# Kernel tuning notes

Measured on AMD Instinct MI355X. Metric: run time of the kernel, lower is better.

The kernel has to match this reference:

```python
import jax, jax.numpy as jnp
import numpy as np

N_NODES = 100000
N_EDGES = 1600000
F_IN = 100
HEADS = 3
HEAD_DIM = 64
HIDDEN = HEADS * HEAD_DIM  # 192
NUM_GRAPHS = 128
NUM_CLASSES = 2
NEG_SLOPE_ATT = 0.2   # PyG GATConv attention leaky_relu slope
NEG_SLOPE_ACT = 0.01  # F.leaky_relu default slope


def setup_inputs() -> dict:
    key = jax.random.key(0)
    ks = jax.random.split(key, 9)
    x = jax.random.normal(ks[0], (N_NODES, F_IN), dtype=jnp.float32)
    edge_index = jax.random.randint(ks[1], (2, N_EDGES), 0, N_NODES, dtype=jnp.int64)
    batch = jnp.sort(jax.random.randint(ks[2], (N_NODES,), 0, NUM_GRAPHS, dtype=jnp.int64))
    s = 0.05
    W = jax.random.normal(ks[3], (F_IN, HIDDEN), dtype=jnp.float32) * s
    att_src = jax.random.normal(ks[4], (HEADS, HEAD_DIM), dtype=jnp.float32) * s
    att_dst = jax.random.normal(ks[5], (HEADS, HEAD_DIM), dtype=jnp.float32) * s
    bias = jax.random.normal(ks[6], (HIDDEN,), dtype=jnp.float32) * s
    cls_W = jax.random.normal(ks[7], (HIDDEN, NUM_CLASSES), dtype=jnp.float32) * s
    cls_b = jax.random.normal(ks[8], (NUM_CLASSES,), dtype=jnp.float32) * s
    return {"x": x, "edge_index": edge_index, "batch": batch, "W": W,
            "att_src": att_src, "att_dst": att_dst, "bias": bias,
            "cls_W": cls_W, "cls_b": cls_b}


def _gat_forward(x, edge_index, batch, W, att_src, att_dst, bias, cls_W, cls_b):
    N = x.shape[0]
    # PyG GATConv adds self-loops by default
    loops = jnp.arange(N, dtype=edge_index.dtype)
    src = jnp.concatenate([edge_index[0], loops])
    dst = jnp.concatenate([edge_index[1], loops])

    h = (x @ W).reshape(N, HEADS, HEAD_DIM)          # [N,H,C]
    a_src = jnp.sum(h * att_src, axis=-1)            # [N,H]
    a_dst = jnp.sum(h * att_dst, axis=-1)            # [N,H]

    e = a_src[src] + a_dst[dst]                      # [Etot,H]
    e = jax.nn.leaky_relu(e, NEG_SLOPE_ATT)

    # segment softmax over incoming edges of each destination node
    m = jax.ops.segment_max(e, dst, num_segments=N)  # [N,H]
    e = jnp.exp(e - m[dst])
    denom = jax.ops.segment_sum(e, dst, num_segments=N)
    alpha = e / denom[dst]                           # [Etot,H]

    msg = h[src] * alpha[:, :, None]                 # [Etot,H,C]
    out = jax.ops.segment_sum(msg, dst, num_segments=N).reshape(N, HIDDEN) + bias

    out = jax.nn.leaky_relu(out, NEG_SLOPE_ACT)      # F.leaky_relu (dropout inactive: eval)
    pooled = jax.ops.segment_max(out, batch, num_segments=NUM_GRAPHS)  # global_max_pool
    return pooled @ cls_W + cls_b                    # [NUM_GRAPHS, NUM_CLASSES]


def reference(x, edge_index, batch, W, att_src, att_dst, bias, cls_W, cls_b):
    return _gat_forward(x, edge_index, batch, W, att_src, att_dst, bias, cls_W, cls_b)
```

## Files before the change

kernel.cpp:

```cpp
#include <hip/hip_runtime.h>
#include <math.h>

#define N_NODES   100000
#define N_EDGES   1600000
#define ETOT      1700000
#define F_IN      100
#define HEADS     3
#define HEAD_DIM  64
#define HIDDEN    192
#define NUM_GRAPHS 128
#define NUM_CLASSES 2
#define WT_COLS   208
#define KPAD      128
#define NCHUNK    ((ETOT + 1023) / 1024)
#define DRANGE    (N_NODES / 8)
#define NGEMM     (N_NODES / 32)
#define OSTRIDE   200
#define GAGG      16
#define CAP       64
#define MWIN      40
#define MWIN_SCAT 16
#define NWIN      131
#define MEGA_GRID (NWIN * MWIN)
#define SCAT_PER_CLASS (NWIN * 2)

typedef unsigned short ushort_t;
typedef __attribute__((ext_vector_type(8))) short short8;
typedef __attribute__((ext_vector_type(4))) float floatx4;

__device__ __forceinline__ unsigned f2ord(float f) {
    unsigned u = __float_as_uint(f);
    return (u & 0x80000000u) ? ~u : (u | 0x80000000u);
}
__device__ __forceinline__ float ord2f(unsigned u) {
    return __uint_as_float((u & 0x80000000u) ? (u & 0x7fffffffu) : ~u);
}
__device__ __forceinline__ unsigned bf16rn(float f) {
    unsigned u = __float_as_uint(f);
    return (u + 0x7fffu + ((u >> 16) & 1u)) >> 16;
}
__device__ __forceinline__ int rl_i(int v, int l) {
    return __builtin_amdgcn_readlane(v, l);
}
__device__ __forceinline__ float rl_f(float v, int l) {
    return __uint_as_float((unsigned)__builtin_amdgcn_readlane((int)__float_as_uint(v), l));
}
template<int CTRL>
__device__ __forceinline__ float bfly(float v) {
    int t = __builtin_amdgcn_update_dpp(0, (int)__float_as_uint(v), CTRL, 0xF, 0xF, false);
    return v + __uint_as_float((unsigned)t);
}
#define DPP_XOR1 0xB1
#define DPP_XOR2 0x4E
#define DPP_XOR8 0x128

__global__ __launch_bounds__(256) void k_prep(
        const float* __restrict__ W, const float* __restrict__ att_src,
        const float* __restrict__ att_dst,
        ushort_t* __restrict__ WT_hi, ushort_t* __restrict__ WT_lo) {
    const int c0 = blockIdx.x * 8;
    const int t = threadIdx.x;
    __shared__ float wsv_s[F_IN * 6];
    if (c0 < HIDDEN + 6 && c0 + 8 > HIDDEN) {
        for (int p = t; p < F_IN * 6; p += 256) {
            int k = p / 6, j = p % 6;
            const float* a = (j < 3) ? att_src : att_dst;
            int hh = j % 3;
            float s = 0.f;
            for (int c = 0; c < HEAD_DIM; c++)
                s += W[k * HIDDEN + hh * HEAD_DIM + c] * a[hh * HEAD_DIM + c];
            wsv_s[p] = s;
        }
        __syncthreads();
    }
    for (int idx = t; idx < 8 * KPAD; idx += 256) {
        int col = c0 + (idx >> 7), k = idx & (KPAD - 1);
        float v = 0.f;
        if (k < F_IN) {
            if (col < HIDDEN) v = W[k * HIDDEN + col];
            else if (col < HIDDEN + 6) v = wsv_s[k * 6 + (col - HIDDEN)];
        }
        unsigned hi = bf16rn(v);
        WT_hi[col * KPAD + k] = (ushort_t)hi;
        float lo = v - __uint_as_float(hi << 16);
        WT_lo[col * KPAD + k] = (ushort_t)bf16rn(lo);
    }
}

__global__ __launch_bounds__(256) void k_mega(
        const float* __restrict__ x,
        const ushort_t* __restrict__ WT_hi, const ushort_t* __restrict__ WT_lo,
        ushort_t* __restrict__ hb,
        float* __restrict__ asrc, float* __restrict__ adst,
        const int* __restrict__ ei, int* __restrict__ count,
        int* __restrict__ srcs) {
    __shared__ ushort_t lds[32 * 136 * 2];
    const int tid = threadIdx.x;
    const int r = blockIdx.x % MWIN, w = blockIdx.x / MWIN;

    if (r < MWIN_SCAT) {
        const int cls = r & 7;
        const int ord = w * 2 + (r >> 3);
        const int dlo = cls * DRANGE, dhi = dlo + DRANGE;
        for (int chunk = ord; chunk < NCHUNK; chunk += SCAT_PER_CLASS) {
            const int base = chunk * 1024 + tid;
            int d4[4], s4[4];
#pragma unroll
            for (int q = 0; q < 4; q++) {
                int j = base + q * 256;
                if (j >= ETOT) { d4[q] = -1; s4[q] = 0; continue; }
                d4[q] = (j < N_EDGES) ? ei[N_EDGES + j] : (j - N_EDGES);
                s4[q] = (j < N_EDGES) ? ei[j] : d4[q];
            }
#pragma unroll
            for (int q = 0; q < 4; q++) {
                int d = d4[q];
                if (d < dlo || d >= dhi) continue;
                int pos = atomicAdd(&count[d], 1);
                if (pos < CAP)
                    __builtin_nontemporal_store(s4[q], &srcs[(size_t)d * CAP + pos]);
            }
        }
        return;
    }

    const int tile = w * (MWIN - MWIN_SCAT) + (r - MWIN_SCAT);
    if (tile >= NGEMM) return;
    ushort_t* xs_hi = lds;
    ushort_t* xs_lo = lds + 32 * 136;
    const int base = tile * 32;
    for (int idx = tid; idx < 32 * 14; idx += 256) {
        int row = idx / 14, u = idx % 14;
        *(unsigned*)(xs_hi + row * 136 + 100 + u * 2) = 0u;
        *(unsigned*)(xs_lo + row * 136 + 100 + u * 2) = 0u;
    }
    for (int p = tid; p < 32 * 25; p += 256) {
        int row = p / 25, q = p % 25;
        float4 v = *(const float4*)(x + (size_t)(base + row) * F_IN + q * 4);
        float vv[4] = {v.x, v.y, v.z, v.w};
        ushort_t h4[4], l4[4];
#pragma unroll
        for (int e = 0; e < 4; e++) {
            unsigned hi = bf16rn(vv[e]);
            h4[e] = (ushort_t)hi;
            float lo = vv[e] - __uint_as_float(hi << 16);
            l4[e] = (ushort_t)bf16rn(lo);
        }
        int off = row * 136 + q * 4;
        *(uint2*)(xs_hi + off) = *(uint2*)h4;
        *(uint2*)(xs_lo + off) = *(uint2*)l4;
    }
    __syncthreads();

    const int wid = tid >> 6, l = tid & 63;
    const int row16 = l & 15, g = l >> 4;
    const int NT = (wid == 3) ? 4 : 3;
    const int t0 = wid * 3;

    floatx4 acc[2][4];
#pragma unroll
    for (int m = 0; m < 2; m++)
#pragma unroll
        for (int i = 0; i < 4; i++) acc[m][i] = (floatx4)0.f;

#pragma unroll
    for (int c = 0; c < 4; c++) {
        const int ke = g * 8 + c * 32;
        short8 ah0 = *(const short8*)(xs_hi + row16 * 136 + ke);
        short8 al0 = *(const short8*)(xs_lo + row16 * 136 + ke);
        short8 ah1 = *(const short8*)(xs_hi + (16 + row16) * 136 + ke);
        short8 al1 = *(const short8*)(xs_lo + (16 + row16) * 136 + ke);
#pragma unroll
        for (int ti = 0; ti < 4; ti++) {
            if (ti >= NT) break;
            const int col = (t0 + ti) * 16 + row16;
            short8 bh = *(const short8*)(WT_hi + col * KPAD + ke);
            short8 bl = *(const short8*)(WT_lo + col * KPAD + ke);
            acc[0][ti] = __builtin_amdgcn_mfma_f32_16x16x32_bf16(ah0, bh, acc[0][ti], 0, 0, 0);
            acc[0][ti] = __builtin_amdgcn_mfma_f32_16x16x32_bf16(ah0, bl, acc[0][ti], 0, 0, 0);
            acc[0][ti] = __builtin_amdgcn_mfma_f32_16x16x32_bf16(al0, bh, acc[0][ti], 0, 0, 0);
            acc[1][ti] = __builtin_amdgcn_mfma_f32_16x16x32_bf16(ah1, bh, acc[1][ti], 0, 0, 0);
            acc[1][ti] = __builtin_amdgcn_mfma_f32_16x16x32_bf16(ah1, bl, acc[1][ti], 0, 0, 0);
            acc[1][ti] = __builtin_amdgcn_mfma_f32_16x16x32_bf16(al1, bh, acc[1][ti], 0, 0, 0);
        }
    }

    __syncthreads();

#pragma unroll
    for (int ti = 0; ti < 4; ti++) {
        if (ti >= NT) break;
        const int tile_c = t0 + ti;
        if (tile_c < 12) {
#pragma unroll
            for (int m = 0; m < 2; m++)
#pragma unroll
                for (int rr = 0; rr < 4; rr++) {
                    int node = m * 16 + g * 4 + rr;
                    lds[node * OSTRIDE + tile_c * 16 + row16] =
                        (ushort_t)bf16rn(acc[m][ti][rr]);
                }
        } else if (row16 < 6) {
#pragma unroll
            for (int m = 0; m < 2; m++)
#pragma unroll
                for (int rr = 0; rr < 4; rr++) {
                    int node = base + m * 16 + g * 4 + rr;
                    if (row16 < 3) asrc[node * HEADS + row16] = acc[m][ti][rr];
                    else           adst[node * HEADS + (row16 - 3)] = acc[m][ti][rr];
                }
        }
    }
    __syncthreads();

    uint4* hb4 = (uint4*)(hb + (size_t)base * HIDDEN);
#pragma unroll
    for (int i = 0; i < 3; i++) {
        int q = tid + i * 256;
        int row = q / 24, c8 = q % 24;
        hb4[q] = *(const uint4*)(lds + row * OSTRIDE + c8 * 8);
    }
}

#define GAT_FMA(u, a)                                         \
    do {                                                      \
        acc[0] += (a) * __uint_as_float((u).x << 16);         \
        acc[1] += (a) * __uint_as_float((u).x & 0xffff0000u); \
        acc[2] += (a) * __uint_as_float((u).y << 16);         \
        acc[3] += (a) * __uint_as_float((u).y & 0xffff0000u); \
        acc[4] += (a) * __uint_as_float((u).z << 16);         \
        acc[5] += (a) * __uint_as_float((u).z & 0xffff0000u); \
        acc[6] += (a) * __uint_as_float((u).w << 16);         \
        acc[7] += (a) * __uint_as_float((u).w & 0xffff0000u); \
        dpart += (a);                                         \
    } while (0)

__global__ __launch_bounds__(192) void k_aggr(const int* __restrict__ count,
        const int* __restrict__ srcs, const float* __restrict__ asrc,
        const float* __restrict__ adst, const ushort_t* __restrict__ hb,
        const float* __restrict__ bias, const int* __restrict__ batch,
        unsigned* __restrict__ pooled) {
    __shared__ float sm[HIDDEN];
    const int n0 = blockIdx.x * GAGG;
    const int tid = threadIdx.x;
    const int head = tid >> 6, lane = tid & 63;
    const int srci = (lane & 3) | ((lane >> 1) & 4);
    const int slot = ((lane >> 2) & 1) | ((lane >> 3) & 6);
    const char* hbase = (const char*)hb + head * 128 + slot * 16;
    const int c0 = head * HEAD_DIM + slot * 8;

    int cntv = (lane < GAGG) ? count[n0 + lane] : 0;
    int bgv  = (lane < GAGG) ? batch[n0 + lane] : 0;
    float adv = (lane < GAGG * HEADS) ? adst[n0 * HEADS + lane] : 0.f;
    float bv[8];
#pragma unroll
    for (int k = 0; k < 8; k++) bv[k] = bias[c0 + k];

    float vmax[8];
#pragma unroll
    for (int k = 0; k < 8; k++) vmax[k] = -INFINITY;
    int curg = rl_i(bgv, 0);

    int cnt_cur = rl_i(cntv, 0); if (cnt_cur > CAP) cnt_cur = CAP;
    int cntB = (GAGG > 1) ? rl_i(cntv, 1) : 0; if (cntB > CAP) cntB = CAP;
    int sA = 0, sB = 0;
    if (lane < cnt_cur)
        sA = __builtin_nontemporal_load(&srcs[(size_t)n0 * CAP + lane]);
    if (lane < cntB)
        sB = __builtin_nontemporal_load(&srcs[(size_t)(n0 + 1) * CAP + lane]);
    float aA = (lane < cnt_cur) ? asrc[sA * HEADS + head] : 0.f;

    for (int g = 0; g < GAGG; g++) {
        const int gg = rl_i(bgv, g);
        if (gg != curg) {
            if ((lane & 11) == 0) {
#pragma unroll
                for (int k = 0; k < 8; k++) sm[c0 + k] = vmax[k];
            }
            __syncthreads();
            atomicMax(&pooled[curg * HIDDEN + tid], f2ord(sm[tid]));
            __syncthreads();
#pragma unroll
            for (int k = 0; k < 8; k++) vmax[k] = -INFINITY;
            curg = gg;
        }

        const int cnt = cnt_cur;
        const float ad = rl_f(adv, g * HEADS + head);

        int cntC = 0, sC = 0;
        if (g + 2 < GAGG) {
            cntC = rl_i(cntv, g + 2); if (cntC > CAP) cntC = CAP;
            if (lane < cntC)
                sC = __builtin_nontemporal_load(&srcs[(size_t)(n0 + g + 2) * CAP + lane]);
        }
        float aB = 0.f;
        if (g + 1 < GAGG && lane < cntB) aB = asrc[sB * HEADS + head];

        float myexp = 0.f; int myoff = 0;
        if (lane < cnt) {
            float e = aA + ad;
            e = (e > 0.f) ? e : 0.2f * e;
            myexp = __expf(e);
            myoff = sA * (HIDDEN * 2);
        }

        float acc[8];
#pragma unroll
        for (int k = 0; k < 8; k++) acc[k] = 0.f;
        float dpart = 0.f;
        const int groups = (cnt + 7) >> 3;
        const int g4 = (groups > 4) ? 4 : groups;

        float av[4]; int ov[4]; uint4 uv[4];
#pragma unroll
        for (int j = 0; j < 4; j++) {
            if (j < g4) {
                int sl = j * 8 + srci;
                av[j] = __shfl(myexp, sl);
                ov[j] = __shfl(myoff, sl);
                uv[j] = *(const uint4*)(hbase + ov[j]);
            }
        }
#pragma unroll
        for (int j = 0; j < 4; j++) {
            if (j < g4) GAT_FMA(uv[j], av[j]);
        }
        for (int j = 4; j < groups; j++) {
            int sl = j * 8 + srci;
            float a   = __shfl(myexp, sl);
            int   off = __shfl(myoff, sl);
            uint4 u = *(const uint4*)(hbase + off);
            GAT_FMA(u, a);
        }

        dpart = bfly<DPP_XOR1>(dpart);
        dpart = bfly<DPP_XOR2>(dpart);
        dpart = bfly<DPP_XOR8>(dpart);
#pragma unroll
        for (int k = 0; k < 8; k++) {
            acc[k] = bfly<DPP_XOR1>(acc[k]);
            acc[k] = bfly<DPP_XOR2>(acc[k]);
            acc[k] = bfly<DPP_XOR8>(acc[k]);
        }

        const float inv = 1.f / dpart;
#pragma unroll
        for (int k = 0; k < 8; k++) {
            float v = acc[k] * inv + bv[k];
            v = (v > 0.f) ? v : 0.01f * v;
            vmax[k] = fmaxf(vmax[k], v);
        }

        sA = sB; sB = sC; aA = aB; cnt_cur = cntB; cntB = cntC;
    }

    if ((lane & 11) == 0) {
#pragma unroll
        for (int k = 0; k < 8; k++) sm[c0 + k] = vmax[k];
    }
    __syncthreads();
    atomicMax(&pooled[curg * HIDDEN + tid], f2ord(sm[tid]));
}

__global__ __launch_bounds__(64) void k_cls(const unsigned* __restrict__ pooled,
        const float* __restrict__ clsW, const float* __restrict__ clsb,
        float* __restrict__ out) {
    const int g = blockIdx.x, lane = threadIdx.x;
    float s0 = 0.f, s1 = 0.f;
#pragma unroll
    for (int i = 0; i < 3; i++) {
        int f = i * 64 + lane;
        float pv = ord2f(pooled[g * HIDDEN + f]);
        s0 += pv * clsW[f * NUM_CLASSES];
        s1 += pv * clsW[f * NUM_CLASSES + 1];
    }
#pragma unroll
    for (int m = 1; m < 64; m <<= 1) {
        s0 += __shfl_xor(s0, m);
        s1 += __shfl_xor(s1, m);
    }
    if (lane == 0) {
        out[g * NUM_CLASSES]     = s0 + clsb[0];
        out[g * NUM_CLASSES + 1] = s1 + clsb[1];
    }
}

extern "C" void kernel_launch(void* const* d_in, const int* in_sizes, int n_in,
                              void* d_out, int out_size, void* d_ws, size_t ws_size,
                              hipStream_t stream) {
    const float* x       = (const float*)d_in[0];
    const int*   ei      = (const int*)d_in[1];
    const int*   batch   = (const int*)d_in[2];
    const float* W       = (const float*)d_in[3];
    const float* att_src = (const float*)d_in[4];
    const float* att_dst = (const float*)d_in[5];
    const float* bias    = (const float*)d_in[6];
    const float* clsW    = (const float*)d_in[7];
    const float* clsb    = (const float*)d_in[8];
    float* out = (float*)d_out;

    char* p = (char*)d_ws;
    auto alloc = [&](size_t bytes) {
        char* r = p; p += (bytes + 255) & ~size_t(255); return r;
    };
    ushort_t* hb     = (ushort_t*)alloc(sizeof(ushort_t) * N_NODES * HIDDEN);
    float*    asrc   = (float*)   alloc(sizeof(float) * N_NODES * HEADS);
    float*    adst   = (float*)   alloc(sizeof(float) * N_NODES * HEADS);
    int*      count  = (int*)     alloc(sizeof(int) * N_NODES);
    int*      srcs   = (int*)     alloc(sizeof(int) * (size_t)N_NODES * CAP);
    ushort_t* WT_hi  = (ushort_t*)alloc(sizeof(ushort_t) * WT_COLS * KPAD);
    ushort_t* WT_lo  = (ushort_t*)alloc(sizeof(ushort_t) * WT_COLS * KPAD);
    unsigned* pooled = (unsigned*)alloc(sizeof(unsigned) * NUM_GRAPHS * HIDDEN);

    hipMemsetAsync(count, 0, sizeof(int) * N_NODES, stream);
    hipMemsetAsync(pooled, 0, sizeof(unsigned) * NUM_GRAPHS * HIDDEN, stream);

    k_prep<<<WT_COLS / 8, 256, 0, stream>>>(W, att_src, att_dst, WT_hi, WT_lo);
    k_mega<<<MEGA_GRID, 256, 0, stream>>>(x, WT_hi, WT_lo, hb, asrc, adst,
                                          ei, count, srcs);
    k_aggr<<<N_NODES / GAGG, 192, 0, stream>>>(count, srcs, asrc, adst, hb, bias,
                                               batch, pooled);
    k_cls<<<NUM_GRAPHS, 64, 0, stream>>>(pooled, clsW, clsb, out);
}
```

Measured before the change: 337.6 us.

## Single-pass edge scatter, packed float2 FMA, and doubled nodes per aggregation block

The edge-scatter blocks now each handle one 1024-edge chunk and cover all destinations, instead of eight destination-range classes that each re-read the whole edge list. The per-edge bf16 accumulate uses float2 vector ops so the compiler can emit packed FMA instructions. The aggregation kernel processes 32 nodes per block instead of 16, so adst is loaded into two lane registers. The risk is more atomic contention on the count array and less locality of srcs writes, since destinations are no longer partitioned, plus fewer aggregation blocks to fill the device.

```diff
diff --git a/kernel.cpp b/kernel.cpp
--- a/kernel.cpp
+++ b/kernel.cpp
@@ -13,20 +13,19 @@
 #define WT_COLS   208
 #define KPAD      128
 #define NCHUNK    ((ETOT + 1023) / 1024)
-#define DRANGE    (N_NODES / 8)
 #define NGEMM     (N_NODES / 32)
 #define OSTRIDE   200
-#define GAGG      16
+#define GAGG      32
 #define CAP       64
 #define MWIN      40
-#define MWIN_SCAT 16
-#define NWIN      131
+#define MWIN_SCAT 14
+#define NWIN      121
 #define MEGA_GRID (NWIN * MWIN)
-#define SCAT_PER_CLASS (NWIN * 2)
 
 typedef unsigned short ushort_t;
 typedef __attribute__((ext_vector_type(8))) short short8;
 typedef __attribute__((ext_vector_type(4))) float floatx4;
+typedef __attribute__((ext_vector_type(2))) float float2v;
 
 __device__ __forceinline__ unsigned f2ord(float f) {
     unsigned u = __float_as_uint(f);
@@ -99,27 +98,24 @@
     const int r = blockIdx.x % MWIN, w = blockIdx.x / MWIN;
 
     if (r < MWIN_SCAT) {
-        const int cls = r & 7;
-        const int ord = w * 2 + (r >> 3);
-        const int dlo = cls * DRANGE, dhi = dlo + DRANGE;
-        for (int chunk = ord; chunk < NCHUNK; chunk += SCAT_PER_CLASS) {
-            const int base = chunk * 1024 + tid;
-            int d4[4], s4[4];
-#pragma unroll
-            for (int q = 0; q < 4; q++) {
-                int j = base + q * 256;
-                if (j >= ETOT) { d4[q] = -1; s4[q] = 0; continue; }
-                d4[q] = (j < N_EDGES) ? ei[N_EDGES + j] : (j - N_EDGES);
-                s4[q] = (j < N_EDGES) ? ei[j] : d4[q];
-            }
-#pragma unroll
-            for (int q = 0; q < 4; q++) {
-                int d = d4[q];
-                if (d < dlo || d >= dhi) continue;
-                int pos = atomicAdd(&count[d], 1);
-                if (pos < CAP)
-                    __builtin_nontemporal_store(s4[q], &srcs[(size_t)d * CAP + pos]);
-            }
+        const int chunk = w * MWIN_SCAT + r;
+        if (chunk >= NCHUNK) return;
+        const int base = chunk * 1024 + tid;
+        int d4[4], s4[4];
+#pragma unroll
+        for (int q = 0; q < 4; q++) {
+            int j = base + q * 256;
+            if (j >= ETOT) { d4[q] = -1; s4[q] = 0; continue; }
+            d4[q] = (j < N_EDGES) ? ei[N_EDGES + j] : (j - N_EDGES);
+            s4[q] = (j < N_EDGES) ? ei[j] : d4[q];
+        }
+#pragma unroll
+        for (int q = 0; q < 4; q++) {
+            int d = d4[q];
+            if (d < 0) continue;
+            int pos = atomicAdd(&count[d], 1);
+            if (pos < CAP)
+                __builtin_nontemporal_store(s4[q], &srcs[(size_t)d * CAP + pos]);
         }
         return;
     }
@@ -222,17 +218,22 @@
     }
 }
 
-#define GAT_FMA(u, a)                                         \
-    do {                                                      \
-        acc[0] += (a) * __uint_as_float((u).x << 16);         \
-        acc[1] += (a) * __uint_as_float((u).x & 0xffff0000u); \
-        acc[2] += (a) * __uint_as_float((u).y << 16);         \
-        acc[3] += (a) * __uint_as_float((u).y & 0xffff0000u); \
-        acc[4] += (a) * __uint_as_float((u).z << 16);         \
-        acc[5] += (a) * __uint_as_float((u).z & 0xffff0000u); \
-        acc[6] += (a) * __uint_as_float((u).w << 16);         \
-        acc[7] += (a) * __uint_as_float((u).w & 0xffff0000u); \
-        dpart += (a);                                         \
+#define GAT_FMA(u, a)                                               \
+    do {                                                            \
+        float2v h0, h1, h2, h3;                                     \
+        h0.x = __uint_as_float((u).x << 16);                        \
+        h0.y = __uint_as_float((u).x & 0xffff0000u);                \
+        h1.x = __uint_as_float((u).y << 16);                        \
+        h1.y = __uint_as_float((u).y & 0xffff0000u);                \
+        h2.x = __uint_as_float((u).z << 16);                        \
+        h2.y = __uint_as_float((u).z & 0xffff0000u);                \
+        h3.x = __uint_as_float((u).w << 16);                        \
+        h3.y = __uint_as_float((u).w & 0xffff0000u);                \
+        acc2[0] += h0 * (a);                                        \
+        acc2[1] += h1 * (a);                                        \
+        acc2[2] += h2 * (a);                                        \
+        acc2[3] += h3 * (a);                                        \
+        dpart += (a);                                               \
     } while (0)
 
 __global__ __launch_bounds__(192) void k_aggr(const int* __restrict__ count,
@@ -251,7 +252,8 @@
 
     int cntv = (lane < GAGG) ? count[n0 + lane] : 0;
     int bgv  = (lane < GAGG) ? batch[n0 + lane] : 0;
-    float adv = (lane < GAGG * HEADS) ? adst[n0 * HEADS + lane] : 0.f;
+    float adv0 = adst[n0 * HEADS + lane];
+    float adv1 = (lane < GAGG * HEADS - 64) ? adst[n0 * HEADS + 64 + lane] : 0.f;
     float bv[8];
 #pragma unroll
     for (int k = 0; k < 8; k++) bv[k] = bias[c0 + k];
@@ -262,7 +264,7 @@
     int curg = rl_i(bgv, 0);
 
     int cnt_cur = rl_i(cntv, 0); if (cnt_cur > CAP) cnt_cur = CAP;
-    int cntB = (GAGG > 1) ? rl_i(cntv, 1) : 0; if (cntB > CAP) cntB = CAP;
+    int cntB = rl_i(cntv, 1); if (cntB > CAP) cntB = CAP;
     int sA = 0, sB = 0;
     if (lane < cnt_cur)
         sA = __builtin_nontemporal_load(&srcs[(size_t)n0 * CAP + lane]);
@@ -286,7 +288,8 @@
         }
 
         const int cnt = cnt_cur;
-        const float ad = rl_f(adv, g * HEADS + head);
+        const int adi = g * HEADS + head;
+        const float ad = (adi < 64) ? rl_f(adv0, adi) : rl_f(adv1, adi - 64);
 
         int cntC = 0, sC = 0;
         if (g + 2 < GAGG) {
@@ -305,9 +308,9 @@
             myoff = sA * (HIDDEN * 2);
         }
 
-        float acc[8];
-#pragma unroll
-        for (int k = 0; k < 8; k++) acc[k] = 0.f;
+        float2v acc2[4];
+#pragma unroll
+        for (int k = 0; k < 4; k++) acc2[k] = (float2v)0.f;
         float dpart = 0.f;
         const int groups = (cnt + 7) >> 3;
         const int g4 = (groups > 4) ? 4 : groups;
@@ -333,6 +336,10 @@
             uint4 u = *(const uint4*)(hbase + off);
             GAT_FMA(u, a);
         }
+
+        float acc[8];
+#pragma unroll
+        for (int k = 0; k < 4; k++) { acc[2 * k] = acc2[k].x; acc[2 * k + 1] = acc2[k].y; }
 
         dpart = bfly<DPP_XOR1>(dpart);
         dpart = bfly<DPP_XOR2>(dpart);
```

Result: no change. 335.5 us (-0.6%).
